# Kernel optimization log

Measured on AMD Instinct MI355X. Metric: run time of the kernel, lower is better.

## Reference

```python
import jax, jax.numpy as jnp
import numpy as np

VOCAB = 20
HID = 128
ACT = 3
IN_DIM = VOCAB + 3
NUM_GRAPHS = 64
N_P, E_P = 100000, 1600000
N_M, E_M = 50000, 800000


def _gcn_conv(x, src, dst, W, b, n_nodes):
    deg = jax.ops.segment_sum(jnp.ones(src.shape[0], x.dtype), dst, num_segments=n_nodes) + 1.0
    dinv = jax.lax.rsqrt(deg)
    xw = x @ W                                    # [N, out]
    coef = dinv[src] * dinv[dst]                  # [E]
    agg = jax.ops.segment_sum(xw[src] * coef[:, None], dst, num_segments=n_nodes)
    # self-loop contribution: norm = dinv[i]*dinv[i] = 1/deg[i]
    return agg + xw / deg[:, None] + b


def _mean_pool(x, batch, n_graphs):
    s = jax.ops.segment_sum(x, batch, num_segments=n_graphs)
    cnt = jax.ops.segment_sum(jnp.ones(x.shape[0], x.dtype), batch, num_segments=n_graphs)
    return s / jnp.maximum(cnt, 1.0)[:, None]


def setup_inputs() -> dict:
    key = jax.random.key(0)
    ks = jax.random.split(key, 24)
    d = {}
    d['residue_p'] = jax.random.randint(ks[0], (N_P,), 0, VOCAB)
    d['pos_p'] = jax.random.normal(ks[1], (N_P, 3), jnp.float32)
    d['edge_index_p'] = jax.random.randint(ks[2], (2, E_P), 0, N_P)
    d['batch_p'] = jnp.sort(jax.random.randint(ks[3], (N_P,), 0, NUM_GRAPHS))
    d['residue_m'] = jax.random.randint(ks[4], (N_M,), 0, VOCAB)
    d['pos_m'] = jax.random.normal(ks[5], (N_M, 3), jnp.float32)
    d['edge_index_m'] = jax.random.randint(ks[6], (2, E_M), 0, N_M)
    d['batch_m'] = jnp.sort(jax.random.randint(ks[7], (N_M,), 0, NUM_GRAPHS))
    s = 0.05
    d['W_p1'] = jax.random.normal(ks[8], (IN_DIM, HID), jnp.float32) * s
    d['b_p1'] = jnp.zeros((HID,), jnp.float32)
    d['W_p2'] = jax.random.normal(ks[9], (HID, HID), jnp.float32) * s
    d['b_p2'] = jnp.zeros((HID,), jnp.float32)
    d['W_m1'] = jax.random.normal(ks[10], (IN_DIM, HID), jnp.float32) * s
    d['b_m1'] = jnp.zeros((HID,), jnp.float32)
    d['W_m2'] = jax.random.normal(ks[11], (HID, HID), jnp.float32) * s
    d['b_m2'] = jnp.zeros((HID,), jnp.float32)
    d['W1'] = jax.random.normal(ks[12], (2 * HID, HID), jnp.float32) * s
    d['b1'] = jnp.zeros((HID,), jnp.float32)
    d['W2'] = jax.random.normal(ks[13], (HID, ACT), jnp.float32) * s
    d['b2'] = jnp.zeros((ACT,), jnp.float32)
    return d


def reference(residue_p, pos_p, edge_index_p, batch_p,
              residue_m, pos_m, edge_index_m, batch_m,
              W_p1, b_p1, W_p2, b_p2, W_m1, b_m1, W_m2, b_m2,
              W1, b1, W2, b2):
    # protein branch
    x_p = jnp.concatenate([jax.nn.one_hot(residue_p, VOCAB, dtype=jnp.float32), pos_p], axis=1)
    sp, dp = edge_index_p[0], edge_index_p[1]
    x_p = jax.nn.relu(_gcn_conv(x_p, sp, dp, W_p1, b_p1, N_P))
    x_p = jax.nn.relu(_gcn_conv(x_p, sp, dp, W_p2, b_p2, N_P))
    protein_embedding = _mean_pool(x_p, batch_p, NUM_GRAPHS)  # [G, HID]
    # micromolecule branch
    x_m = jnp.concatenate([jax.nn.one_hot(residue_m, VOCAB, dtype=jnp.float32), pos_m], axis=1)
    sm, dm = edge_index_m[0], edge_index_m[1]
    x_m = jax.nn.relu(_gcn_conv(x_m, sm, dm, W_m1, b_m1, N_M))
    x_m = jax.nn.relu(_gcn_conv(x_m, sm, dm, W_m2, b_m2, N_M))
    # inject protein context per micromolecule node
    ctx = protein_embedding[batch_m]                # [N_M, HID]
    feat = jnp.concatenate([x_m, ctx], axis=1)      # [N_M, 2*HID]
    h = jax.nn.relu(feat @ W1 + b1)
    return h @ W2 + b2                              # [N_M, ACT]
```

## Files before the change

### kernel.cpp

```cpp
#include <hip/hip_runtime.h>
#include <hip/hip_bf16.h>
#include <hip/hip_fp16.h>

#define HID 128
#define BIN_T 8192
#define NBMAX 1664
#define CAP 2560

typedef _Float16 f16;
typedef __attribute__((ext_vector_type(2))) _Float16 f16x2;
typedef __attribute__((ext_vector_type(4))) _Float16 f16x4;
typedef __attribute__((ext_vector_type(8))) _Float16 f16x8;
typedef __attribute__((ext_vector_type(4))) float f32x4;



__global__ void k_prep_all(const float* __restrict__ Wp2, const float* __restrict__ Wm2,
                           const float* __restrict__ W1,
                           f16* __restrict__ Wp2t, f16* __restrict__ Wm2t,
                           f16* __restrict__ W1at,
                           int* __restrict__ bcur_p, int* __restrict__ bcur_m,
                           const int* __restrict__ batch_p, int* __restrict__ pcnt,
                           float* __restrict__ psum, int N_P) {
    int idx = blockIdx.x * 256 + threadIdx.x;
    if (idx < 16384) {
        int n = idx & 127, k = idx >> 7;
        Wp2t[n * 128 + k] = (f16)Wp2[k * 128 + n];
        Wm2t[n * 128 + k] = (f16)Wm2[k * 128 + n];
        W1at[n * 128 + k] = (f16)W1[k * 128 + n];
    }
    if (idx <= NBMAX) { bcur_p[idx] = idx * CAP; bcur_m[idx] = idx * CAP; }
    if (idx < 64 * HID) psum[idx] = 0.f;
    if (idx < 64) {
        int g = idx;
        int lo = 0, hi = N_P;
        while (lo < hi) { int mid = (lo + hi) >> 1; if (batch_p[mid] < g) lo = mid + 1; else hi = mid; }
        int a = lo;
        lo = 0; hi = N_P;
        while (lo < hi) { int mid = (lo + hi) >> 1; if (batch_p[mid] < g + 1) lo = mid + 1; else hi = mid; }
        pcnt[g] = lo - a;
    }
}


__global__ void k_tile_bin2(const int* __restrict__ src_p, const int* __restrict__ dst_p,
                            int* __restrict__ bcur_p, unsigned int* __restrict__ pairs_p,
                            int E_p, int NB_p, int TP,
                            const int* __restrict__ src_m, const int* __restrict__ dst_m,
                            int* __restrict__ bcur_m, unsigned int* __restrict__ pairs_m,
                            int E_m, int NB_m) {
    __shared__ unsigned int dbuf[BIN_T];
    __shared__ unsigned short perm[BIN_T];
    __shared__ int hist[NBMAX];
    __shared__ int lbase[NBMAX];
    __shared__ int gbase[NBMAX];
    __shared__ int tt[256];
    bool isP = (int)blockIdx.x < TP;
    const int* src = isP ? src_p : src_m;
    const int* dst = isP ? dst_p : dst_m;
    int* bcursor = isP ? bcur_p : bcur_m;
    unsigned int* pairs = isP ? pairs_p : pairs_m;
    int E = isP ? E_p : E_m;
    int NB = isP ? NB_p : NB_m;
    int tilebase = (isP ? blockIdx.x : blockIdx.x - TP) * BIN_T;
    int t = threadIdx.x;
    int n = min(BIN_T, E - tilebase);
    for (int i = t; i < NB; i += 256) hist[i] = 0;
    __syncthreads();
    for (int i = t; i < n; i += 256) {
        unsigned int d = (unsigned int)dst[tilebase + i];
        dbuf[i] = d;
        atomicAdd(&hist[d >> 6], 1);
    }
    __syncthreads();
    {
        int b0 = t * 7, loc[7], run = 0;
        #pragma unroll
        for (int k = 0; k < 7; ++k) {
            int b = b0 + k;
            int c = (b < NB) ? hist[b] : 0;
            loc[k] = run; run += c;
        }
        tt[t] = run;
        __syncthreads();
        int val = run;
        for (int off = 1; off < 256; off <<= 1) {
            int add = (t >= off) ? tt[t - off] : 0;
            __syncthreads();
            tt[t] += add;
            __syncthreads();
        }
        int ebase = tt[t] - val;
        #pragma unroll
        for (int k = 0; k < 7; ++k) {
            int b = b0 + k;
            if (b < NB) lbase[b] = ebase + loc[k];
        }
    }
    __syncthreads();
    for (int i = t; i < NB; i += 256) {
        int c = hist[i];
        gbase[i] = (c > 0) ? atomicAdd(&bcursor[i], c) : 0;
    }
    __syncthreads();
    for (int i = t; i < NB; i += 256) hist[i] = lbase[i];
    __syncthreads();
    for (int i = t; i < n; i += 256) {
        int b = (int)(dbuf[i] >> 6);
        int p = atomicAdd(&hist[b], 1);
        perm[p] = (unsigned short)i;
    }
    __syncthreads();
    for (int p = t; p < n; p += 256) {
        int li = perm[p];
        unsigned int d = dbuf[li];
        int b = (int)(d >> 6);
        int addr = gbase[b] + (p - lbase[b]);
        pairs[addr] = (unsigned int)src[tilebase + li] | ((d & 63u) << 26);
    }
}


__global__ void k_fill_a(
        const unsigned int* __restrict__ pairs_p, const int* __restrict__ bcur_p,
        const int* __restrict__ res_p, const float* __restrict__ pos_p,
        int4* __restrict__ rec16_p, float* __restrict__ dinv_p,
        int* __restrict__ rowptr_p, int* __restrict__ rowend_p, int* __restrict__ csr_p,
        int N_p, int NB_p,
        const unsigned int* __restrict__ pairs_m, const int* __restrict__ bcur_m,
        const int* __restrict__ res_m, const float* __restrict__ pos_m,
        int4* __restrict__ rec16_m, float* __restrict__ dinv_m,
        int* __restrict__ rowptr_m, int* __restrict__ rowend_m, int* __restrict__ csr_m,
        int N_m) {
    __shared__ int cnt[64];
    __shared__ int cur[64];
    bool isP = (int)blockIdx.x < NB_p;
    const unsigned int* pairs = isP ? pairs_p : pairs_m;
    const int* bcur = isP ? bcur_p : bcur_m;
    const int* residue = isP ? res_p : res_m;
    const float* pos = isP ? pos_p : pos_m;
    int4* rec16 = isP ? rec16_p : rec16_m;
    float* dinvA = isP ? dinv_p : dinv_m;
    int* rowptr = isP ? rowptr_p : rowptr_m;
    int* rowend = isP ? rowend_p : rowend_m;
    int* csr_src = isP ? csr_p : csr_m;
    int N = isP ? N_p : N_m;
    int b = isP ? blockIdx.x : blockIdx.x - NB_p;
    int t = threadIdx.x, base = b * 64;
    if (t < 64) cnt[t] = 0;
    __syncthreads();
    int lo = b * CAP, hi = bcur[b];
    for (int e = lo + t; e < hi; e += 256)
        atomicAdd(&cnt[pairs[e] >> 26], 1);
    __syncthreads();
    if (t < 64) {
        int off = 0;
        for (int k = 0; k < t; ++k) off += cnt[k];
        int node = base + t;
        if (node < N) {
            rowptr[node] = lo + off;
            rowend[node] = lo + off + cnt[t];
            float d = (float)cnt[t] + 1.0f;
            float di = 1.0f / sqrtf(d);
            dinvA[node] = di;
            float px = pos[node * 3 + 0], py = pos[node * 3 + 1], pz = pos[node * 3 + 2];
            f16x4 r;
            r[0] = (f16)di; r[1] = (f16)(di * px); r[2] = (f16)(di * py); r[3] = (f16)(di * pz);
            int4 rc;
            rc.x = ((const int*)&r)[0];
            rc.y = ((const int*)&r)[1];
            rc.z = residue[node];
            rc.w = 0;
            rec16[node] = rc;
        }
        cur[t] = lo + off;
    }
    __syncthreads();
    for (int e = lo + t; e < hi; e += 256) {
        unsigned int pk = pairs[e];
        int slot = atomicAdd(&cur[pk >> 26], 1);
        csr_src[slot] = (int)(pk & 0x1FFFFu);
    }
}


__global__ __launch_bounds__(256) void k_l1(
        const unsigned int* __restrict__ pairs_p, const int* __restrict__ bcur_p,
        const int4* __restrict__ rec16_p,
        const float* __restrict__ W_p, const float* __restrict__ bias_p,
        const float* __restrict__ dinv_p, f16* __restrict__ y1_p, int N_p, int NB_p,
        const unsigned int* __restrict__ pairs_m, const int* __restrict__ bcur_m,
        const int4* __restrict__ rec16_m,
        const float* __restrict__ W_m, const float* __restrict__ bias_m,
        const float* __restrict__ dinv_m, f16* __restrict__ y1_m, int N_m) {
    __shared__ float acc[64][25];
    __shared__ float sdv[64];
    bool isP = (int)blockIdx.x < NB_p;
    const unsigned int* pairs = isP ? pairs_p : pairs_m;
    const int* bcur = isP ? bcur_p : bcur_m;
    const int4* rec16 = isP ? rec16_p : rec16_m;
    const float* W = isP ? W_p : W_m;
    const float* bias = isP ? bias_p : bias_m;
    const float* dinvA = isP ? dinv_p : dinv_m;
    f16* y1h = isP ? y1_p : y1_m;
    int N = isP ? N_p : N_m;
    int b = isP ? blockIdx.x : blockIdx.x - NB_p;
    int t = threadIdx.x, base = b * 64;
    for (int q = t; q < 64 * 25; q += 256) ((float*)acc)[q] = 0.f;
    if (t < 64 && base + t < N) sdv[t] = dinvA[base + t];
    int jj = (t & 63) * 2, slot = t >> 6;
    float wreg[23][2];
    #pragma unroll
    for (int k = 0; k < 23; ++k) {
        float2 wv = *(const float2*)&W[k * 128 + jj];
        wreg[k][0] = wv.x; wreg[k][1] = wv.y;
    }
    __syncthreads();
    int lo = b * CAP, hi = bcur[b];
    for (int e = lo + t; e < hi; e += 1024) {
        unsigned int pk[4];
        int4 rc[4];
        bool hv[4];
        #pragma unroll
        for (int u = 0; u < 4; ++u) {
            int ee = e + u * 256;
            hv[u] = ee < hi;
            pk[u] = pairs[hv[u] ? ee : e];
        }
        #pragma unroll
        for (int u = 0; u < 4; ++u)
            rc[u] = rec16[pk[u] & 0x1FFFFu];
        #pragma unroll
        for (int u = 0; u < 4; ++u) {
            if (!hv[u]) continue;
            f16x2 lo2 = *(const f16x2*)&rc[u].x;
            f16x2 hi2 = *(const f16x2*)&rc[u].y;
            int dl = (int)(pk[u] >> 26);
            int rs = rc[u].z;
            atomicAdd(&acc[dl][rs], (float)lo2[0]);
            atomicAdd(&acc[dl][20], (float)lo2[1]);
            atomicAdd(&acc[dl][21], (float)hi2[0]);
            atomicAdd(&acc[dl][22], (float)hi2[1]);
        }
    }
    __syncthreads();
    if (t < 64) {
        int node = base + t;
        if (node < N) {
            int4 rc = rec16[node];
            f16x2 lo2 = *(const f16x2*)&rc.x;
            f16x2 hi2 = *(const f16x2*)&rc.y;
            acc[t][rc.z] += (float)lo2[0];
            acc[t][20] += (float)lo2[1];
            acc[t][21] += (float)hi2[0];
            acc[t][22] += (float)hi2[1];
            float di = sdv[t];
            #pragma unroll
            for (int k = 0; k < 23; ++k) acc[t][k] *= di;
        }
    }
    __syncthreads();
    float bj0 = bias[jj], bj1 = bias[jj + 1];
    for (int r = slot * 16; r < slot * 16 + 16; ++r) {
        int node = base + r;
        if (node >= N) break;
        float a0 = bj0, a1 = bj1;
        #pragma unroll
        for (int k = 0; k < 23; ++k) {
            float zv = acc[r][k];
            a0 += zv * wreg[k][0];
            a1 += zv * wreg[k][1];
        }
        float dv = sdv[r];
        f16x2 o;
        o[0] = (f16)(fmaxf(a0, 0.f) * dv);
        o[1] = (f16)(fmaxf(a1, 0.f) * dv);
        *(f16x2*)&y1h[(size_t)node * HID + jj] = o;
    }
}


#define AGG16_TO_LDS(zs, sidx, y1h, rowptr, rowend, csr_src, dinvA, N)          \
    {                                                                           \
        int sp0 = rowptr[tile];                                                 \
        int sp1 = rowend[min(tile + 15, N - 1)];                                \
        int slen = sp1 - sp0;                                                   \
        for (int i = t; i < slen; i += 256) sidx[i] = csr_src[sp0 + i];         \
        __syncthreads();                                                        \
        for (int i = 0; i < 4; ++i) {                                           \
            int node = tile + w * 4 + i;                                        \
            int cn = min(node, N - 1);                                          \
            int lb = rowptr[cn] - sp0, le = rowend[cn] - sp0;                   \
            float fa[8] = {};                                                   \
            int e = lb;                                                         \
            for (; e + 8 <= le; e += 8) {                                       \
                int i0 = sidx[e + kb], i1 = sidx[e + 4 + kb];                   \
                f16x8 v0 = *(const f16x8*)(y1h + (size_t)i0 * HID + lr * 8);    \
                f16x8 v1 = *(const f16x8*)(y1h + (size_t)i1 * HID + lr * 8);    \
                _Pragma("unroll")                                               \
                for (int j = 0; j < 8; ++j)                                     \
                    fa[j] += (float)v0[j] + (float)v1[j];                       \
            }                                                                   \
            if (e + 4 <= le) {                                                  \
                int i0 = sidx[e + kb];                                          \
                f16x8 v0 = *(const f16x8*)(y1h + (size_t)i0 * HID + lr * 8);    \
                _Pragma("unroll")                                               \
                for (int j = 0; j < 8; ++j) fa[j] += (float)v0[j];              \
                e += 4;                                                         \
            }                                                                   \
            if (e + kb < le) {                                                  \
                int i0 = sidx[e + kb];                                          \
                f16x8 v0 = *(const f16x8*)(y1h + (size_t)i0 * HID + lr * 8);    \
                _Pragma("unroll")                                               \
                for (int j = 0; j < 8; ++j) fa[j] += (float)v0[j];              \
            }                                                                   \
            _Pragma("unroll")                                                   \
            for (int j = 0; j < 8; ++j) {                                       \
                fa[j] += __shfl_xor(fa[j], 16);                                 \
                fa[j] += __shfl_xor(fa[j], 32);                                 \
            }                                                                   \
            if (kb == 0) {                                                      \
                f16x8 sv = *(const f16x8*)(y1h + (size_t)cn * HID + lr * 8);    \
                float di = dinvA[cn];                                           \
                f16x8 o;                                                        \
                _Pragma("unroll")                                               \
                for (int j = 0; j < 8; ++j)                                     \
                    o[j] = (f16)((fa[j] + (float)sv[j]) * di);                  \
                *(f16x8*)&zs[w * 4 + i][lr * 8] = o;                            \
            }                                                                   \
        }                                                                       \
    }                                                                           \
    __syncthreads();


__global__ __launch_bounds__(256) void k_agg_combined(
        const f16* __restrict__ y1p, const int* __restrict__ rpp, const int* __restrict__ rep,
        const int* __restrict__ csrp, const float* __restrict__ dvp,
        const f16* __restrict__ Wp2t, const float* __restrict__ bp2,
        const int* __restrict__ batchp, float* __restrict__ psum, int Np, int PB,
        const f16* __restrict__ y1m, const int* __restrict__ rpm, const int* __restrict__ rem,
        const int* __restrict__ csrm, const float* __restrict__ dvm,
        const f16* __restrict__ Wm2t, const float* __restrict__ bm2,
        f16* __restrict__ x2g, int Nm) {
    __shared__ __attribute__((aligned(16))) f16 zs[16][136];
    __shared__ int sidx[CAP];
    int t = threadIdx.x, lane = t & 63, w = t >> 6;
    int lr = lane & 15, kb = lane >> 4;
    bool isP = (int)blockIdx.x < PB;
    if (isP) {
        const f16* y1h = y1p;
        int N = Np;
        int tile = blockIdx.x * 16;
        AGG16_TO_LDS(zs, sidx, y1h, rpp, rep, csrp, dvp, N)
        int g0 = batchp[min(tile, N - 1)];
        bool uni = (tile + 15 < N) && (g0 == batchp[tile + 15]);
        int gr[4]; bool val[4];
        if (!uni) {
            #pragma unroll
            for (int r = 0; r < 4; ++r) {
                int row = tile + kb * 4 + r;
                val[r] = row < N;
                gr[r] = batchp[min(row, N - 1)];
            }
        }
        f16x8 afr[4];
        #pragma unroll
        for (int kc = 0; kc < 4; ++kc)
            afr[kc] = *(const f16x8*)&zs[lr][kc * 32 + kb * 8];
        #pragma unroll
        for (int q = 0; q < 2; ++q) {
            int ct = w * 2 + q;
            f32x4 c4 = {0.f, 0.f, 0.f, 0.f};
            int col = ct * 16 + lr;
            const f16* wp = Wp2t + (size_t)col * HID + kb * 8;
            #pragma unroll
            for (int kc = 0; kc < 4; ++kc) {
                f16x8 bf = *(const f16x8*)(wp + kc * 32);
                c4 = __builtin_amdgcn_mfma_f32_16x16x32_f16(afr[kc], bf, c4, 0, 0, 0);
            }
            float bj = bp2[col];
            if (uni) {
                float ps = 0.f;
                #pragma unroll
                for (int r = 0; r < 4; ++r) ps += fmaxf(c4[r] + bj, 0.f);
                ps += __shfl_xor(ps, 16);
                ps += __shfl_xor(ps, 32);
                if (kb == 0) atomicAdd(&psum[g0 * HID + col], ps);
            } else {
                #pragma unroll
                for (int r = 0; r < 4; ++r)
                    if (val[r]) atomicAdd(&psum[gr[r] * HID + col], fmaxf(c4[r] + bj, 0.f));
            }
        }
    } else {
        const f16* y1h = y1m;
        int N = Nm;
        int tile = (blockIdx.x - PB) * 16;
        AGG16_TO_LDS(zs, sidx, y1h, rpm, rem, csrm, dvm, N)
        f16x8 afr[4];
        #pragma unroll
        for (int kc = 0; kc < 4; ++kc)
            afr[kc] = *(const f16x8*)&zs[lr][kc * 32 + kb * 8];
        __syncthreads();
        #pragma unroll
        for (int q = 0; q < 2; ++q) {
            int ct = w * 2 + q;
            f32x4 c4 = {0.f, 0.f, 0.f, 0.f};
            int col = ct * 16 + lr;
            const f16* wp = Wm2t + (size_t)col * HID + kb * 8;
            #pragma unroll
            for (int kc = 0; kc < 4; ++kc) {
                f16x8 bf = *(const f16x8*)(wp + kc * 32);
                c4 = __builtin_amdgcn_mfma_f32_16x16x32_f16(afr[kc], bf, c4, 0, 0, 0);
            }
            float bj = bm2[col];
            #pragma unroll
            for (int r = 0; r < 4; ++r)
                zs[kb * 4 + r][col] = (f16)fmaxf(c4[r] + bj, 0.f);
        }
        __syncthreads();
        int row = t >> 4, c8 = (t & 15) * 8;
        if (tile + row < N)
            *(f16x8*)&x2g[(size_t)(tile + row) * HID + c8] = *(const f16x8*)&zs[row][c8];
    }
}

__global__ void k_ctxw_div(const float* __restrict__ psum, const int* __restrict__ pcnt,
                           const float* __restrict__ W1, const float* __restrict__ b1,
                           float* __restrict__ ctxW) {
    __shared__ float pr[128];
    int g = blockIdx.x, j = threadIdx.x;
    pr[j] = psum[g * HID + j] / fmaxf((float)pcnt[g], 1.f);
    __syncthreads();
    float a = b1[j];
    #pragma unroll 4
    for (int k = 0; k < HID; ++k) a += pr[k] * W1[(HID + k) * HID + j];
    ctxW[g * HID + j] = a;
}

__global__ __launch_bounds__(256) void k_mm_finish(
        const f16* __restrict__ x2g, const int* __restrict__ batch,
        const float* __restrict__ ctxW, const f16* __restrict__ W1at,
        const float* __restrict__ W2, const float* __restrict__ b2,
        float* __restrict__ out, int N) {
    __shared__ float part[4][16][3];
    int tile = blockIdx.x * 16;
    int t = threadIdx.x, lane = t & 63, w = t >> 6;
    int lr = lane & 15, kb = lane >> 4;
    int cr = min(tile + lr, N - 1);
    f16x8 afr[4];
    #pragma unroll
    for (int kc = 0; kc < 4; ++kc)
        afr[kc] = *(const f16x8*)&x2g[(size_t)cr * HID + kc * 32 + kb * 8];
    int gidx[4];
    #pragma unroll
    for (int r = 0; r < 4; ++r)
        gidx[r] = batch[min(tile + kb * 4 + r, N - 1)];
    float po[4][3] = {};
    #pragma unroll
    for (int q = 0; q < 2; ++q) {
        int ct = w * 2 + q;
        f32x4 c4 = {0.f, 0.f, 0.f, 0.f};
        int col = ct * 16 + lr;
        const f16* wp = W1at + (size_t)col * HID + kb * 8;
        #pragma unroll
        for (int kc = 0; kc < 4; ++kc) {
            f16x8 bf = *(const f16x8*)(wp + kc * 32);
            c4 = __builtin_amdgcn_mfma_f32_16x16x32_f16(afr[kc], bf, c4, 0, 0, 0);
        }
        float w0 = W2[col * 3 + 0], w1 = W2[col * 3 + 1], w2 = W2[col * 3 + 2];
        #pragma unroll
        for (int r = 0; r < 4; ++r) {
            float h = fmaxf(c4[r] + ctxW[gidx[r] * HID + col], 0.f);
            po[r][0] += h * w0;
            po[r][1] += h * w1;
            po[r][2] += h * w2;
        }
    }
    #pragma unroll
    for (int m = 1; m < 16; m <<= 1) {
        #pragma unroll
        for (int r = 0; r < 4; ++r) {
            po[r][0] += __shfl_xor(po[r][0], m);
            po[r][1] += __shfl_xor(po[r][1], m);
            po[r][2] += __shfl_xor(po[r][2], m);
        }
    }
    if (lr == 0) {
        #pragma unroll
        for (int r = 0; r < 4; ++r) {
            part[w][kb * 4 + r][0] = po[r][0];
            part[w][kb * 4 + r][1] = po[r][1];
            part[w][kb * 4 + r][2] = po[r][2];
        }
    }
    __syncthreads();
    if (t < 48) {
        int row = t / 3, c = t - row * 3;
        int gr2 = tile + row;
        if (gr2 < N)
            out[(size_t)gr2 * 3 + c] = part[0][row][c] + part[1][row][c] +
                                       part[2][row][c] + part[3][row][c] + b2[c];
    }
}


extern "C" void kernel_launch(void* const* d_in, const int* in_sizes, int n_in,
                              void* d_out, int out_size, void* d_ws, size_t ws_size,
                              hipStream_t stream) {
    const int*   residue_p = (const int*)d_in[0];
    const float* pos_p     = (const float*)d_in[1];
    const int*   ei_p      = (const int*)d_in[2];
    const int*   batch_p   = (const int*)d_in[3];
    const int*   residue_m = (const int*)d_in[4];
    const float* pos_m     = (const float*)d_in[5];
    const int*   ei_m      = (const int*)d_in[6];
    const int*   batch_m   = (const int*)d_in[7];
    const float* W_p1 = (const float*)d_in[8];
    const float* b_p1 = (const float*)d_in[9];
    const float* W_p2 = (const float*)d_in[10];
    const float* b_p2 = (const float*)d_in[11];
    const float* W_m1 = (const float*)d_in[12];
    const float* b_m1 = (const float*)d_in[13];
    const float* W_m2 = (const float*)d_in[14];
    const float* b_m2 = (const float*)d_in[15];
    const float* W1   = (const float*)d_in[16];
    const float* b1   = (const float*)d_in[17];
    const float* W2   = (const float*)d_in[18];
    const float* b2   = (const float*)d_in[19];

    const int N_P = in_sizes[0];
    const int E_P = in_sizes[2] / 2;
    const int N_M = in_sizes[4];
    const int E_M = in_sizes[6] / 2;
    const int G = 64;
    const int NB_P = (N_P + 63) / 64;
    const int NB_M = (N_M + 63) / 64;
    const int PB = (N_P + 15) / 16;
    const int MB = (N_M + 15) / 16;

    char* ws = (char*)d_ws;
    size_t off = 0;
    auto alloc = [&](size_t bytes) {
        char* p = ws + off;
        off += (bytes + 511) & ~size_t(511);
        return p;
    };
    f16*           y1_p    = (f16*)  alloc((size_t)N_P * HID * 2);
    f16*           y1_m    = (f16*)  alloc((size_t)N_M * HID * 2);
    f16*           x2g     = (f16*)  alloc((size_t)N_M * HID * 2);
    int4*          rec16_p = (int4*) alloc((size_t)N_P * 16);
    int4*          rec16_m = (int4*) alloc((size_t)N_M * 16);
    float*         dinv_p  = (float*)alloc((size_t)N_P * 4);
    float*         dinv_m  = (float*)alloc((size_t)N_M * 4);
    int*           rp_p    = (int*)  alloc((size_t)N_P * 4);
    int*           rp_m    = (int*)  alloc((size_t)N_M * 4);
    int*           re_p    = (int*)  alloc((size_t)N_P * 4);
    int*           re_m    = (int*)  alloc((size_t)N_M * 4);
    int*           bcur_p  = (int*)  alloc((NBMAX + 1) * 4);
    int*           bcur_m  = (int*)  alloc((NBMAX + 1) * 4);
    unsigned int*  prs_p   = (unsigned int*)alloc((size_t)NB_P * CAP * 4);
    unsigned int*  prs_m   = (unsigned int*)alloc((size_t)NB_M * CAP * 4);
    int*           csr_p   = (int*)  alloc((size_t)NB_P * CAP * 4);
    int*           csr_m   = (int*)  alloc((size_t)NB_M * CAP * 4);
    float*         psum    = (float*)alloc((size_t)G * HID * 4);
    int*           pcnt    = (int*)  alloc((size_t)G * 4);
    float*         ctxW    = (float*)alloc((size_t)G * HID * 4);
    f16*           Wp2t    = (f16*)  alloc(128 * 128 * 2);
    f16*           Wm2t    = (f16*)  alloc(128 * 128 * 2);
    f16*           W1at    = (f16*)  alloc(128 * 128 * 2);

    const int TP = (E_P + BIN_T - 1) / BIN_T;
    const int TM = (E_M + BIN_T - 1) / BIN_T;

    k_prep_all<<<64, 256, 0, stream>>>(W_p2, W_m2, W1, Wp2t, Wm2t, W1at,
                                       bcur_p, bcur_m, batch_p, pcnt, psum, N_P);
    k_tile_bin2<<<TP + TM, 256, 0, stream>>>(ei_p, ei_p + E_P, bcur_p, prs_p, E_P, NB_P, TP,
                                             ei_m, ei_m + E_M, bcur_m, prs_m, E_M, NB_M);
    k_fill_a<<<NB_P + NB_M, 256, 0, stream>>>(
        prs_p, bcur_p, residue_p, pos_p, rec16_p, dinv_p, rp_p, re_p, csr_p, N_P, NB_P,
        prs_m, bcur_m, residue_m, pos_m, rec16_m, dinv_m, rp_m, re_m, csr_m, N_M);
    k_l1<<<NB_P + NB_M, 256, 0, stream>>>(
        prs_p, bcur_p, rec16_p, W_p1, b_p1, dinv_p, y1_p, N_P, NB_P,
        prs_m, bcur_m, rec16_m, W_m1, b_m1, dinv_m, y1_m, N_M);
    k_agg_combined<<<PB + MB, 256, 0, stream>>>(
        y1_p, rp_p, re_p, csr_p, dinv_p, Wp2t, b_p2, batch_p, psum, N_P, PB,
        y1_m, rp_m, re_m, csr_m, dinv_m, Wm2t, b_m2, x2g, N_M);
    k_ctxw_div<<<G, HID, 0, stream>>>(psum, pcnt, W1, b1, ctxW);
    k_mm_finish<<<MB, 256, 0, stream>>>(x2g, batch_m, ctxW, W1at, W2, b2,
                                        (float*)d_out, N_M);
}
```

Measured before the change: 270.0 us.

## Pack source residue into CSR entries and aggregate layer-1 by destination row

The binning kernel now looks up each source node's residue and packs it into bits 17-21 of the edge word, so the per-node record shrinks from 16 to 8 bytes. Layer 1 now walks the CSR rows with four threads per destination. The three position features are summed in registers and combined with shuffles, so only the one-hot slot still uses an LDS atomic. The layer-2 aggregation gets a 16-wide unrolled gather, and the shared index buffer shrinks to 1024 entries with a fallback to global reads for large tiles. The cost is an extra random residue gather per edge during binning.

```diff
diff --git a/kernel.cpp b/kernel.cpp
--- a/kernel.cpp
+++ b/kernel.cpp
@@ -6,6 +6,7 @@
 #define BIN_T 8192
 #define NBMAX 1664
 #define CAP 2560
+#define SIDX 1024
 
 typedef _Float16 f16;
 typedef __attribute__((ext_vector_type(2))) _Float16 f16x2;
@@ -44,9 +45,11 @@
 
 
 __global__ void k_tile_bin2(const int* __restrict__ src_p, const int* __restrict__ dst_p,
+                            const int* __restrict__ res_p,
                             int* __restrict__ bcur_p, unsigned int* __restrict__ pairs_p,
                             int E_p, int NB_p, int TP,
                             const int* __restrict__ src_m, const int* __restrict__ dst_m,
+                            const int* __restrict__ res_m,
                             int* __restrict__ bcur_m, unsigned int* __restrict__ pairs_m,
                             int E_m, int NB_m) {
     __shared__ unsigned int dbuf[BIN_T];
@@ -58,6 +61,7 @@
     bool isP = (int)blockIdx.x < TP;
     const int* src = isP ? src_p : src_m;
     const int* dst = isP ? dst_p : dst_m;
+    const int* res = isP ? res_p : res_m;
     int* bcursor = isP ? bcur_p : bcur_m;
     unsigned int* pairs = isP ? pairs_p : pairs_m;
     int E = isP ? E_p : E_m;
@@ -116,20 +120,21 @@
         unsigned int d = dbuf[li];
         int b = (int)(d >> 6);
         int addr = gbase[b] + (p - lbase[b]);
-        pairs[addr] = (unsigned int)src[tilebase + li] | ((d & 63u) << 26);
+        int sv = src[tilebase + li];
+        pairs[addr] = (unsigned int)sv | ((unsigned int)res[sv] << 17) | ((d & 63u) << 26);
     }
 }
 
 
 __global__ void k_fill_a(
         const unsigned int* __restrict__ pairs_p, const int* __restrict__ bcur_p,
-        const int* __restrict__ res_p, const float* __restrict__ pos_p,
-        int4* __restrict__ rec16_p, float* __restrict__ dinv_p,
+        const float* __restrict__ pos_p,
+        f16x4* __restrict__ rec8_p, float* __restrict__ dinv_p,
         int* __restrict__ rowptr_p, int* __restrict__ rowend_p, int* __restrict__ csr_p,
         int N_p, int NB_p,
         const unsigned int* __restrict__ pairs_m, const int* __restrict__ bcur_m,
-        const int* __restrict__ res_m, const float* __restrict__ pos_m,
-        int4* __restrict__ rec16_m, float* __restrict__ dinv_m,
+        const float* __restrict__ pos_m,
+        f16x4* __restrict__ rec8_m, float* __restrict__ dinv_m,
         int* __restrict__ rowptr_m, int* __restrict__ rowend_m, int* __restrict__ csr_m,
         int N_m) {
     __shared__ int cnt[64];
@@ -137,9 +142,8 @@
     bool isP = (int)blockIdx.x < NB_p;
     const unsigned int* pairs = isP ? pairs_p : pairs_m;
     const int* bcur = isP ? bcur_p : bcur_m;
-    const int* residue = isP ? res_p : res_m;
     const float* pos = isP ? pos_p : pos_m;
-    int4* rec16 = isP ? rec16_p : rec16_m;
+    f16x4* rec8 = isP ? rec8_p : rec8_m;
     float* dinvA = isP ? dinv_p : dinv_m;
     int* rowptr = isP ? rowptr_p : rowptr_m;
     int* rowend = isP ? rowend_p : rowend_m;
@@ -166,12 +170,7 @@
             float px = pos[node * 3 + 0], py = pos[node * 3 + 1], pz = pos[node * 3 + 2];
             f16x4 r;
             r[0] = (f16)di; r[1] = (f16)(di * px); r[2] = (f16)(di * py); r[3] = (f16)(di * pz);
-            int4 rc;
-            rc.x = ((const int*)&r)[0];
-            rc.y = ((const int*)&r)[1];
-            rc.z = residue[node];
-            rc.w = 0;
-            rec16[node] = rc;
+            rec8[node] = r;
         }
         cur[t] = lo + off;
     }
@@ -179,26 +178,30 @@
     for (int e = lo + t; e < hi; e += 256) {
         unsigned int pk = pairs[e];
         int slot = atomicAdd(&cur[pk >> 26], 1);
-        csr_src[slot] = (int)(pk & 0x1FFFFu);
+        csr_src[slot] = (int)(pk & 0x3FFFFFu);
     }
 }
 
 
 __global__ __launch_bounds__(256) void k_l1(
-        const unsigned int* __restrict__ pairs_p, const int* __restrict__ bcur_p,
-        const int4* __restrict__ rec16_p,
+        const int* __restrict__ csr_p, const int* __restrict__ rowptr_p,
+        const int* __restrict__ rowend_p, const f16x4* __restrict__ rec8_p,
+        const int* __restrict__ res_p,
         const float* __restrict__ W_p, const float* __restrict__ bias_p,
         const float* __restrict__ dinv_p, f16* __restrict__ y1_p, int N_p, int NB_p,
-        const unsigned int* __restrict__ pairs_m, const int* __restrict__ bcur_m,
-        const int4* __restrict__ rec16_m,
+        const int* __restrict__ csr_m, const int* __restrict__ rowptr_m,
+        const int* __restrict__ rowend_m, const f16x4* __restrict__ rec8_m,
+        const int* __restrict__ res_m,
         const float* __restrict__ W_m, const float* __restrict__ bias_m,
         const float* __restrict__ dinv_m, f16* __restrict__ y1_m, int N_m) {
     __shared__ float acc[64][25];
     __shared__ float sdv[64];
     bool isP = (int)blockIdx.x < NB_p;
-    const unsigned int* pairs = isP ? pairs_p : pairs_m;
-    const int* bcur = isP ? bcur_p : bcur_m;
-    const int4* rec16 = isP ? rec16_p : rec16_m;
+    const int* csr = isP ? csr_p : csr_m;
+    const int* rowptr = isP ? rowptr_p : rowptr_m;
+    const int* rowend = isP ? rowend_p : rowend_m;
+    const f16x4* rec8 = isP ? rec8_p : rec8_m;
+    const int* residue = isP ? res_p : res_m;
     const float* W = isP ? W_p : W_m;
     const float* bias = isP ? bias_p : bias_m;
     const float* dinvA = isP ? dinv_p : dinv_m;
@@ -206,7 +209,7 @@
     int N = isP ? N_p : N_m;
     int b = isP ? blockIdx.x : blockIdx.x - NB_p;
     int t = threadIdx.x, base = b * 64;
-    for (int q = t; q < 64 * 25; q += 256) ((float*)acc)[q] = 0.f;
+    for (int q2 = t; q2 < 64 * 25; q2 += 256) ((float*)acc)[q2] = 0.f;
     if (t < 64 && base + t < N) sdv[t] = dinvA[base + t];
     int jj = (t & 63) * 2, slot = t >> 6;
     float wreg[23][2];
@@ -216,44 +219,47 @@
         wreg[k][0] = wv.x; wreg[k][1] = wv.y;
     }
     __syncthreads();
-    int lo = b * CAP, hi = bcur[b];
-    for (int e = lo + t; e < hi; e += 1024) {
-        unsigned int pk[4];
-        int4 rc[4];
-        bool hv[4];
-        #pragma unroll
-        for (int u = 0; u < 4; ++u) {
-            int ee = e + u * 256;
-            hv[u] = ee < hi;
-            pk[u] = pairs[hv[u] ? ee : e];
-        }
-        #pragma unroll
-        for (int u = 0; u < 4; ++u)
-            rc[u] = rec16[pk[u] & 0x1FFFFu];
-        #pragma unroll
-        for (int u = 0; u < 4; ++u) {
-            if (!hv[u]) continue;
-            f16x2 lo2 = *(const f16x2*)&rc[u].x;
-            f16x2 hi2 = *(const f16x2*)&rc[u].y;
-            int dl = (int)(pk[u] >> 26);
-            int rs = rc[u].z;
-            atomicAdd(&acc[dl][rs], (float)lo2[0]);
-            atomicAdd(&acc[dl][20], (float)lo2[1]);
-            atomicAdd(&acc[dl][21], (float)hi2[0]);
-            atomicAdd(&acc[dl][22], (float)hi2[1]);
+    {
+        int nl = t >> 2, q = t & 3;
+        int node = base + nl;
+        int cn = min(node, N - 1);
+        int lb = rowptr[cn], le = rowend[cn];
+        float f20 = 0.f, f21 = 0.f, f22 = 0.f;
+        int e = lb + q;
+        for (; e + 4 < le; e += 8) {
+            unsigned int c0 = (unsigned int)csr[e];
+            unsigned int c1 = (unsigned int)csr[e + 4];
+            f16x4 r0 = rec8[c0 & 0x1FFFFu];
+            f16x4 r1 = rec8[c1 & 0x1FFFFu];
+            atomicAdd(&acc[nl][(c0 >> 17) & 31u], (float)r0[0]);
+            f20 += (float)r0[1]; f21 += (float)r0[2]; f22 += (float)r0[3];
+            atomicAdd(&acc[nl][(c1 >> 17) & 31u], (float)r1[0]);
+            f20 += (float)r1[1]; f21 += (float)r1[2]; f22 += (float)r1[3];
+        }
+        if (e < le) {
+            unsigned int c0 = (unsigned int)csr[e];
+            f16x4 r0 = rec8[c0 & 0x1FFFFu];
+            atomicAdd(&acc[nl][(c0 >> 17) & 31u], (float)r0[0]);
+            f20 += (float)r0[1]; f21 += (float)r0[2]; f22 += (float)r0[3];
+        }
+        f20 += __shfl_xor(f20, 1); f20 += __shfl_xor(f20, 2);
+        f21 += __shfl_xor(f21, 1); f21 += __shfl_xor(f21, 2);
+        f22 += __shfl_xor(f22, 1); f22 += __shfl_xor(f22, 2);
+        if (q == 0 && node < N) {
+            acc[nl][20] = f20;
+            acc[nl][21] = f21;
+            acc[nl][22] = f22;
         }
     }
     __syncthreads();
     if (t < 64) {
         int node = base + t;
         if (node < N) {
-            int4 rc = rec16[node];
-            f16x2 lo2 = *(const f16x2*)&rc.x;
-            f16x2 hi2 = *(const f16x2*)&rc.y;
-            acc[t][rc.z] += (float)lo2[0];
-            acc[t][20] += (float)lo2[1];
-            acc[t][21] += (float)hi2[0];
-            acc[t][22] += (float)hi2[1];
+            f16x4 r = rec8[node];
+            acc[t][residue[node]] += (float)r[0];
+            acc[t][20] += (float)r[1];
+            acc[t][21] += (float)r[2];
+            acc[t][22] += (float)r[3];
             float di = sdv[t];
             #pragma unroll
             for (int k = 0; k < 23; ++k) acc[t][k] *= di;
@@ -285,16 +291,34 @@
         int sp0 = rowptr[tile];                                                 \
         int sp1 = rowend[min(tile + 15, N - 1)];                                \
         int slen = sp1 - sp0;                                                   \
-        for (int i = t; i < slen; i += 256) sidx[i] = csr_src[sp0 + i];         \
+        bool staged = slen <= SIDX;                                             \
+        if (staged)                                                             \
+            for (int i = t; i < slen; i += 256) sidx[i] = csr_src[sp0 + i];     \
         __syncthreads();                                                        \
+        const int* idxp = staged ? sidx : (csr_src + sp0);                      \
         for (int i = 0; i < 4; ++i) {                                           \
             int node = tile + w * 4 + i;                                        \
             int cn = min(node, N - 1);                                          \
             int lb = rowptr[cn] - sp0, le = rowend[cn] - sp0;                   \
             float fa[8] = {};                                                   \
             int e = lb;                                                         \
+            for (; e + 16 <= le; e += 16) {                                     \
+                int i0 = idxp[e + kb] & 0x1FFFF;                                \
+                int i1 = idxp[e + 4 + kb] & 0x1FFFF;                            \
+                int i2 = idxp[e + 8 + kb] & 0x1FFFF;                            \
+                int i3 = idxp[e + 12 + kb] & 0x1FFFF;                           \
+                f16x8 v0 = *(const f16x8*)(y1h + (size_t)i0 * HID + lr * 8);    \
+                f16x8 v1 = *(const f16x8*)(y1h + (size_t)i1 * HID + lr * 8);    \
+                f16x8 v2 = *(const f16x8*)(y1h + (size_t)i2 * HID + lr * 8);    \
+                f16x8 v3 = *(const f16x8*)(y1h + (size_t)i3 * HID + lr * 8);    \
+                _Pragma("unroll")                                               \
+                for (int j = 0; j < 8; ++j)                                     \
+                    fa[j] += ((float)v0[j] + (float)v1[j]) +                    \
+                             ((float)v2[j] + (float)v3[j]);                     \
+            }                                                                   \
             for (; e + 8 <= le; e += 8) {                                       \
-                int i0 = sidx[e + kb], i1 = sidx[e + 4 + kb];                   \
+                int i0 = idxp[e + kb] & 0x1FFFF;                                \
+                int i1 = idxp[e + 4 + kb] & 0x1FFFF;                            \
                 f16x8 v0 = *(const f16x8*)(y1h + (size_t)i0 * HID + lr * 8);    \
                 f16x8 v1 = *(const f16x8*)(y1h + (size_t)i1 * HID + lr * 8);    \
                 _Pragma("unroll")                                               \
@@ -302,14 +326,14 @@
                     fa[j] += (float)v0[j] + (float)v1[j];                       \
             }                                                                   \
             if (e + 4 <= le) {                                                  \
-                int i0 = sidx[e + kb];                                          \
+                int i0 = idxp[e + kb] & 0x1FFFF;                                \
                 f16x8 v0 = *(const f16x8*)(y1h + (size_t)i0 * HID + lr * 8);    \
                 _Pragma("unroll")                                               \
                 for (int j = 0; j < 8; ++j) fa[j] += (float)v0[j];              \
                 e += 4;                                                         \
             }                                                                   \
             if (e + kb < le) {                                                  \
-                int i0 = sidx[e + kb];                                          \
+                int i0 = idxp[e + kb] & 0x1FFFF;                                \
                 f16x8 v0 = *(const f16x8*)(y1h + (size_t)i0 * HID + lr * 8);    \
                 _Pragma("unroll")                                               \
                 for (int j = 0; j < 8; ++j) fa[j] += (float)v0[j];              \
@@ -343,7 +367,7 @@
         const f16* __restrict__ Wm2t, const float* __restrict__ bm2,
         f16* __restrict__ x2g, int Nm) {
     __shared__ __attribute__((aligned(16))) f16 zs[16][136];
-    __shared__ int sidx[CAP];
+    __shared__ int sidx[SIDX];
     int t = threadIdx.x, lane = t & 63, w = t >> 6;
     int lr = lane & 15, kb = lane >> 4;
     bool isP = (int)blockIdx.x < PB;
@@ -546,43 +570,45 @@
         off += (bytes + 511) & ~size_t(511);
         return p;
     };
-    f16*           y1_p    = (f16*)  alloc((size_t)N_P * HID * 2);
-    f16*           y1_m    = (f16*)  alloc((size_t)N_M * HID * 2);
-    f16*           x2g     = (f16*)  alloc((size_t)N_M * HID * 2);
-    int4*          rec16_p = (int4*) alloc((size_t)N_P * 16);
-    int4*          rec16_m = (int4*) alloc((size_t)N_M * 16);
-    float*         dinv_p  = (float*)alloc((size_t)N_P * 4);
-    float*         dinv_m  = (float*)alloc((size_t)N_M * 4);
-    int*           rp_p    = (int*)  alloc((size_t)N_P * 4);
-    int*           rp_m    = (int*)  alloc((size_t)N_M * 4);
-    int*           re_p    = (int*)  alloc((size_t)N_P * 4);
-    int*           re_m    = (int*)  alloc((size_t)N_M * 4);
-    int*           bcur_p  = (int*)  alloc((NBMAX + 1) * 4);
-    int*           bcur_m  = (int*)  alloc((NBMAX + 1) * 4);
-    unsigned int*  prs_p   = (unsigned int*)alloc((size_t)NB_P * CAP * 4);
-    unsigned int*  prs_m   = (unsigned int*)alloc((size_t)NB_M * CAP * 4);
-    int*           csr_p   = (int*)  alloc((size_t)NB_P * CAP * 4);
-    int*           csr_m   = (int*)  alloc((size_t)NB_M * CAP * 4);
-    float*         psum    = (float*)alloc((size_t)G * HID * 4);
-    int*           pcnt    = (int*)  alloc((size_t)G * 4);
-    float*         ctxW    = (float*)alloc((size_t)G * HID * 4);
-    f16*           Wp2t    = (f16*)  alloc(128 * 128 * 2);
-    f16*           Wm2t    = (f16*)  alloc(128 * 128 * 2);
-    f16*           W1at    = (f16*)  alloc(128 * 128 * 2);
+    f16*           y1_p   = (f16*)  alloc((size_t)N_P * HID * 2);
+    f16*           y1_m   = (f16*)  alloc((size_t)N_M * HID * 2);
+    f16*           x2g    = (f16*)  alloc((size_t)N_M * HID * 2);
+    f16x4*         rec8_p = (f16x4*)alloc((size_t)N_P * 8);
+    f16x4*         rec8_m = (f16x4*)alloc((size_t)N_M * 8);
+    float*         dinv_p = (float*)alloc((size_t)N_P * 4);
+    float*         dinv_m = (float*)alloc((size_t)N_M * 4);
+    int*           rp_p   = (int*)  alloc((size_t)N_P * 4);
+    int*           rp_m   = (int*)  alloc((size_t)N_M * 4);
+    int*           re_p   = (int*)  alloc((size_t)N_P * 4);
+    int*           re_m   = (int*)  alloc((size_t)N_M * 4);
+    int*           bcur_p = (int*)  alloc((NBMAX + 1) * 4);
+    int*           bcur_m = (int*)  alloc((NBMAX + 1) * 4);
+    unsigned int*  prs_p  = (unsigned int*)alloc((size_t)NB_P * CAP * 4);
+    unsigned int*  prs_m  = (unsigned int*)alloc((size_t)NB_M * CAP * 4);
+    int*           csr_p  = (int*)  alloc((size_t)NB_P * CAP * 4);
+    int*           csr_m  = (int*)  alloc((size_t)NB_M * CAP * 4);
+    float*         psum   = (float*)alloc((size_t)G * HID * 4);
+    int*           pcnt   = (int*)  alloc((size_t)G * 4);
+    float*         ctxW   = (float*)alloc((size_t)G * HID * 4);
+    f16*           Wp2t   = (f16*)  alloc(128 * 128 * 2);
+    f16*           Wm2t   = (f16*)  alloc(128 * 128 * 2);
+    f16*           W1at   = (f16*)  alloc(128 * 128 * 2);
 
     const int TP = (E_P + BIN_T - 1) / BIN_T;
     const int TM = (E_M + BIN_T - 1) / BIN_T;
 
     k_prep_all<<<64, 256, 0, stream>>>(W_p2, W_m2, W1, Wp2t, Wm2t, W1at,
                                        bcur_p, bcur_m, batch_p, pcnt, psum, N_P);
-    k_tile_bin2<<<TP + TM, 256, 0, stream>>>(ei_p, ei_p + E_P, bcur_p, prs_p, E_P, NB_P, TP,
-                                             ei_m, ei_m + E_M, bcur_m, prs_m, E_M, NB_M);
+    k_tile_bin2<<<TP + TM, 256, 0, stream>>>(ei_p, ei_p + E_P, residue_p, bcur_p, prs_p,
+                                             E_P, NB_P, TP,
+                                             ei_m, ei_m + E_M, residue_m, bcur_m, prs_m,
+                                             E_M, NB_M);
     k_fill_a<<<NB_P + NB_M, 256, 0, stream>>>(
-        prs_p, bcur_p, residue_p, pos_p, rec16_p, dinv_p, rp_p, re_p, csr_p, N_P, NB_P,
-        prs_m, bcur_m, residue_m, pos_m, rec16_m, dinv_m, rp_m, re_m, csr_m, N_M);
+        prs_p, bcur_p, pos_p, rec8_p, dinv_p, rp_p, re_p, csr_p, N_P, NB_P,
+        prs_m, bcur_m, pos_m, rec8_m, dinv_m, rp_m, re_m, csr_m, N_M);
     k_l1<<<NB_P + NB_M, 256, 0, stream>>>(
-        prs_p, bcur_p, rec16_p, W_p1, b_p1, dinv_p, y1_p, N_P, NB_P,
-        prs_m, bcur_m, rec16_m, W_m1, b_m1, dinv_m, y1_m, N_M);
+        csr_p, rp_p, re_p, rec8_p, residue_p, W_p1, b_p1, dinv_p, y1_p, N_P, NB_P,
+        csr_m, rp_m, re_m, rec8_m, residue_m, W_m1, b_m1, dinv_m, y1_m, N_M);
     k_agg_combined<<<PB + MB, 256, 0, stream>>>(
         y1_p, rp_p, re_p, csr_p, dinv_p, Wp2t, b_p2, batch_p, psum, N_P, PB,
         y1_m, rp_m, re_m, csr_m, dinv_m, Wm2t, b_m2, x2g, N_M);
```

Result: faster. 241.0 us, median of 2 (-10.7%).
